# Kernel optimization log

Hardware: AMD Instinct MI355X
Metric: run time of the kernel (lower is better)

Reference implementation:

```python
import jax, jax.numpy as jnp
import numpy as np

B, D, E, H, L = 32768, 512, 10, 128, 2  # batch, input_dim, max_charts, expert hidden, latent_dim
RH1, RH2 = 256, 128                      # router hidden sizes
TAU = 3.0


def setup_inputs() -> dict:
    key = jax.random.key(0)
    ks = jax.random.split(key, 16)
    rnd = lambda k, *s: (jax.random.normal(k, s, jnp.float32) * 0.05)
    return {
        "x": jax.random.normal(ks[0], (B, D), jnp.float32),
        "u": jax.random.uniform(ks[1], (B, E), jnp.float32),
        # router params (last layer init ~ N(0, 0.01), bias 0, as in _init_router)
        "rw1": rnd(ks[2], D, RH1), "rb1": jnp.zeros((RH1,), jnp.float32),
        "rw2": rnd(ks[3], RH1, RH2), "rb2": jnp.zeros((RH2,), jnp.float32),
        "rw3": jax.random.normal(ks[4], (RH2, E), jnp.float32) * 0.01,
        "rb3": jnp.zeros((E,), jnp.float32),
        # stacked expert params: all 10 experts batched along leading dim
        "ew1": rnd(ks[5], E, D, H), "eb1": rnd(ks[6], E, H),
        "ew2": rnd(ks[7], E, H, H), "eb2": rnd(ks[8], E, H),
        "ew3": rnd(ks[9], E, H, L), "eb3": rnd(ks[10], E, L),
    }


def reference(x, u, rw1, rb1, rw2, rb2, rw3, rb3, ew1, eb1, ew2, eb2, ew3, eb3):
    # router MLP: D -> 256 -> 128 -> E
    h = jax.nn.relu(x @ rw1 + rb1)
    h = jax.nn.relu(h @ rw2 + rb2)
    logits = h @ rw3 + rb3                                  # [B, E]
    # gumbel_softmax(tau=3.0, hard=False): softmax((logits + gumbel)/tau)
    g = -jnp.log(-jnp.log(jnp.clip(u, 1e-10, 1.0)) + 1e-10)
    weights = jax.nn.softmax((logits + g) / TAU, axis=1)    # [B, E]
    # all 10 experts as batched GEMMs (fuses the python loop over charts)
    h1 = jax.nn.relu(jnp.einsum('bi,eio->beo', x, ew1) + eb1[None])   # [B, E, H]
    h2 = jax.nn.relu(jnp.einsum('beh,eho->beo', h1, ew2) + eb2[None]) # [B, E, H]
    zc = jnp.einsum('beh,ehl->bel', h2, ew3) + eb3[None]              # [B, E, L]
    z = jnp.einsum('be,bel->bl', weights, zc)                         # [B, L]
    chart_outputs = jnp.transpose(zc, (1, 0, 2))                      # [E, B, L]
    return z, weights, chart_outputs
```

## Files before the change

kernel.cpp:

```cpp
#include <hip/hip_runtime.h>
#include <stdint.h>

typedef __bf16 bf16x8 __attribute__((ext_vector_type(8)));
typedef float floatx4 __attribute__((ext_vector_type(4)));
typedef unsigned short ushort_t;

__device__ __forceinline__ ushort_t bf16rne(float f) {
    union { float f; unsigned u; } v; v.f = f;
    return (ushort_t)((v.u + 0x7fffu + ((v.u >> 16) & 1u)) >> 16);
}

__device__ __forceinline__ void gl_lds16(const ushort_t* g, ushort_t* l) {
    __builtin_amdgcn_global_load_lds(
        (const __attribute__((address_space(1))) unsigned int*)g,
        (__attribute__((address_space(3))) unsigned int*)l, 16, 0, 0);
}


#define WAIT_VM_BAR(n)    do { asm volatile("s_waitcnt vmcnt(" #n ")" ::: "memory"); __builtin_amdgcn_s_barrier(); } while (0)
#define WAIT_VM_LG_BAR(n) do { asm volatile("s_waitcnt vmcnt(" #n ") lgkmcnt(0)" ::: "memory"); __builtin_amdgcn_s_barrier(); } while (0)
#define WAIT_LG_BAR()     do { asm volatile("s_waitcnt lgkmcnt(0)" ::: "memory"); __builtin_amdgcn_s_barrier(); } while (0)

__global__ void prep(const float* __restrict__ x, ushort_t* __restrict__ x16,
                     const float* __restrict__ ew1, ushort_t* __restrict__ ew1t,
                     const float* __restrict__ ew2, ushort_t* __restrict__ ew2t,
                     const float* __restrict__ rw1, ushort_t* __restrict__ rw1t,
                     const float* __restrict__ rw2, ushort_t* __restrict__ rw2t) {
    __shared__ ushort_t sT[64 * 65];
    int b = blockIdx.x, tid = threadIdx.x;
    if (b < 16384) {
        int i = b * 256 + tid;
        float4 f = ((const float4*)x)[i];
        union { ushort_t s[4]; uint2 v; } pk;
        pk.s[0] = bf16rne(f.x); pk.s[1] = bf16rne(f.y);
        pk.s[2] = bf16rne(f.z); pk.s[3] = bf16rne(f.w);
        ((uint2*)x16)[i] = pk.v;
        return;
    }
    const float* in; ushort_t* outp; int K, N, k0, n0;
    int i = b - 16384;
    if (i < 160) {
        int e = i >> 4, t = i & 15;
        in = ew1 + e * 65536; outp = ew1t + e * 65536;
        K = 512; N = 128; k0 = (t >> 1) * 64; n0 = (t & 1) * 64;
    } else if (i < 200) {
        i -= 160; int e = i >> 2, t = i & 3;
        in = ew2 + e * 16384; outp = ew2t + e * 16384;
        K = 128; N = 128; k0 = (t >> 1) * 64; n0 = (t & 1) * 64;
    } else if (i < 232) {
        i -= 200; in = rw1; outp = rw1t;
        K = 512; N = 256; k0 = (i >> 2) * 64; n0 = (i & 3) * 64;
    } else {
        i -= 232; in = rw2; outp = rw2t;
        K = 256; N = 128; k0 = (i >> 1) * 64; n0 = (i & 1) * 64;
    }
    {
        int c = tid & 63, r0 = tid >> 6;
#pragma unroll
        for (int p = 0; p < 16; ++p) {
            int r = r0 * 16 + p;
            sT[c * 65 + r] = bf16rne(in[(size_t)(k0 + r) * N + n0 + c]);
        }
        __syncthreads();
        int rr = tid & 63, c0 = tid >> 6;
#pragma unroll
        for (int p = 0; p < 16; ++p) {
            int cc = c0 * 16 + p;
            outp[(size_t)(n0 + cc) * K + k0 + rr] = sT[cc * 65 + rr];
        }
    }
}

__global__ __launch_bounds__(256, 2)
void fused_main(const ushort_t* __restrict__ x16,
                const ushort_t* __restrict__ rw1t, const float* __restrict__ rb1,
                const ushort_t* __restrict__ rw2t, const float* __restrict__ rb2,
                const float* __restrict__ rw3, const float* __restrict__ rb3,
                const float* __restrict__ u,
                const ushort_t* __restrict__ ew1t, const ushort_t* __restrict__ ew2t,
                const float* __restrict__ eb1, const float* __restrict__ eb2,
                const float* __restrict__ ew3, const float* __restrict__ eb3,
                float* __restrict__ wts, float* __restrict__ chart) {
    __shared__ alignas(16) ushort_t sU[24576];
    __shared__ float sB1[2][128];
    __shared__ float sB2[2][128];
    __shared__ float sW3e[2][256];
    __shared__ float zbuf[128][2];

    const int tid = threadIdx.x;
    const int id = blockIdx.x;
    const int wave = tid >> 6, lane = tid & 63;
    const int ln15 = lane & 15, q = lane >> 4;
    const int wm = (wave & 1) * 64, wn = (wave >> 1) * 64;
    const int mhalf = wm >> 6, nhalf = wn >> 6;
    const int rl = lane >> 2, cl = lane & 3;
    const int sw = (cl ^ ((rl >> 1) & 3)) * 8;
    const int rg0 = wave * 2, rg1 = rg0 + 1;
    const int fslot = (4 * ln15 + (q ^ ((ln15 >> 1) & 3))) * 8;

    if (id < 256) {
        const int rb = (id & 7) * 32 + (id >> 3);
        if (tid < 128) sB2[0][tid] = rb2[tid];
        else sB2[1][tid - 128] = rb2[tid];
        const ushort_t* xblk = x16 + (size_t)rb * 128 * 512;

        const ushort_t* w1base = rw1t;
        auto stage_rt = [&](int dst, int k0) {
            gl_lds16(xblk + (size_t)(rg0 * 16 + rl) * 512 + k0 + sw, &sU[dst + rg0 * 512]);
            gl_lds16(xblk + (size_t)(rg1 * 16 + rl) * 512 + k0 + sw, &sU[dst + rg1 * 512]);
            gl_lds16(w1base + (size_t)(rg0 * 16 + rl) * 512 + k0 + sw, &sU[dst + 4096 + rg0 * 512]);
            gl_lds16(w1base + (size_t)(rg1 * 16 + rl) * 512 + k0 + sw, &sU[dst + 4096 + rg1 * 512]);
        };
        auto stage_rw2 = [&](int dst, int kh, int ph) {
#pragma unroll
            for (int r = 0; r < 2; ++r) {
                int s = wave * 2 + r;
                gl_lds16(rw2t + (size_t)(s * 16 + rl) * 256 + ph * 128 + kh * 32 + sw,
                         &sU[dst + s * 512]);
            }
        };

        floatx4 acc2[4][4];
#pragma unroll
        for (int i = 0; i < 4; ++i)
#pragma unroll
            for (int j = 0; j < 4; ++j) acc2[i][j] = (floatx4){0.f, 0.f, 0.f, 0.f};

        auto comp_rg2 = [&](int rbase, int kh) {
            bf16x8 a[4], b[4];
#pragma unroll
            for (int t = 0; t < 4; ++t) a[t] = *(const bf16x8*)(&sU[rbase + (mhalf * 4 + t) * 512 + fslot]);
#pragma unroll
            for (int t = 0; t < 4; ++t) b[t] = *(const bf16x8*)(&sU[8192 + kh * 4096 + (nhalf * 4 + t) * 512 + lane * 8]);
            __builtin_amdgcn_s_setprio(1);
#pragma unroll
            for (int i = 0; i < 4; ++i)
#pragma unroll
                for (int j = 0; j < 4; ++j)
                    acc2[i][j] = __builtin_amdgcn_mfma_f32_16x16x32_bf16(a[i], b[j], acc2[i][j], 0, 0, 0);
            __builtin_amdgcn_s_setprio(0);
        };

        for (int ph = 0; ph < 2; ++ph) {
            w1base = rw1t + (size_t)ph * 65536;
            if (tid < 128) sB1[0][tid] = rb1[ph * 128 + tid];

            floatx4 acc[4][4];
#pragma unroll
            for (int i = 0; i < 4; ++i)
#pragma unroll
                for (int j = 0; j < 4; ++j) acc[i][j] = (floatx4){0.f, 0.f, 0.f, 0.f};

            auto comp_rt = [&](int base) {
                bf16x8 a[4], b[4];
#pragma unroll
                for (int t = 0; t < 4; ++t) a[t] = *(const bf16x8*)(&sU[base + 4096 + (mhalf * 4 + t) * 512 + fslot]);
#pragma unroll
                for (int t = 0; t < 4; ++t) b[t] = *(const bf16x8*)(&sU[base + (nhalf * 4 + t) * 512 + fslot]);
                __builtin_amdgcn_s_setprio(1);
#pragma unroll
                for (int i = 0; i < 4; ++i)
#pragma unroll
                    for (int j = 0; j < 4; ++j)
                        acc[i][j] = __builtin_amdgcn_mfma_f32_16x16x32_bf16(a[i], b[j], acc[i][j], 0, 0, 0);
                __builtin_amdgcn_s_setprio(0);
            };

            stage_rt(0, 0);
#pragma unroll 1
            for (int p = 0; p < 8; ++p) {
                int k0 = p * 64;
                stage_rt(8192, k0 + 32);
                WAIT_VM_BAR(4);
                comp_rt(0);
                WAIT_LG_BAR();
                if (p < 7) {
                    stage_rt(0, k0 + 64);
                    WAIT_VM_BAR(4);
                } else {
                    WAIT_VM_BAR(0);
                }
                comp_rt(8192);
                WAIT_LG_BAR();
            }

            stage_rw2(0, 0, ph);

#pragma unroll
            for (int i = 0; i < 4; ++i) {
                int hbase = wm + 16 * i;
                int kh = hbase >> 5;
                int qhi = (hbase >> 4) & 1;
                int slotq = 2 * qhi + (q >> 1);
                int h0 = hbase + q * 4;
#pragma unroll
                for (int j = 0; j < 4; ++j) {
                    union { ushort_t s[4]; uint2 v; } pk;
#pragma unroll
                    for (int r = 0; r < 4; ++r)
                        pk.s[r] = bf16rne(fmaxf(acc[i][j][r] + sB1[0][h0 + r], 0.f));
                    *(uint2*)(&sU[8192 + kh * 4096 + (nhalf * 4 + j) * 512 + slotq * 128 + ln15 * 8 + (q & 1) * 4]) = pk.v;
                }
            }

            stage_rw2(4096, 1, ph); WAIT_VM_LG_BAR(8); comp_rg2(0, 0);    WAIT_LG_BAR();
            stage_rw2(0, 2, ph);    WAIT_VM_LG_BAR(8); comp_rg2(4096, 1); WAIT_LG_BAR();
            stage_rw2(4096, 3, ph); WAIT_VM_LG_BAR(8); comp_rg2(0, 2);    WAIT_LG_BAR();
            WAIT_VM_LG_BAR(0);                         comp_rg2(4096, 3); WAIT_LG_BAR();
        }

        __syncthreads();
        float* sw3r = (float*)sU;
        float* lgbuf = (float*)(&sU[2560]);
        for (int i = tid; i < 1280; i += 256) sw3r[i] = rw3[i];
        __syncthreads();

        float lg[4][10];
#pragma unroll
        for (int j = 0; j < 4; ++j)
#pragma unroll
            for (int ee = 0; ee < 10; ++ee) lg[j][ee] = 0.f;
#pragma unroll
        for (int i = 0; i < 4; ++i) {
#pragma unroll
            for (int r = 0; r < 4; ++r) {
                int n = wm + i * 16 + q * 4 + r;
                float bias = n < 128 ? sB2[0][n] : sB2[1][n - 128];
                const float* w3r = &sw3r[n * 10];
#pragma unroll
                for (int j = 0; j < 4; ++j) {
                    float val = fmaxf(acc2[i][j][r] + bias, 0.f);
#pragma unroll
                    for (int ee = 0; ee < 10; ++ee) lg[j][ee] += val * w3r[ee];
                }
            }
        }
#pragma unroll
        for (int j = 0; j < 4; ++j)
#pragma unroll
            for (int ee = 0; ee < 10; ++ee) {
                lg[j][ee] += __shfl_xor(lg[j][ee], 16, 64);
                lg[j][ee] += __shfl_xor(lg[j][ee], 32, 64);
            }
        if (wm == 0 && q == 0) {
#pragma unroll
            for (int j = 0; j < 4; ++j) {
                int row = wn + 16 * j + ln15;
#pragma unroll
                for (int ee = 0; ee < 10; ++ee) lgbuf[row * 10 + ee] = lg[j][ee];
            }
        }
        __syncthreads();
        if (wm == 64 && q == 0) {
#pragma unroll
            for (int j = 0; j < 4; ++j) {
                int row = wn + 16 * j + ln15;
#pragma unroll
                for (int ee = 0; ee < 10; ++ee) lgbuf[row * 10 + ee] += lg[j][ee];
            }
        }
        __syncthreads();
        if (tid < 128) {
            int grow = rb * 128 + tid;
            float v[10], mx = -1e30f;
#pragma unroll
            for (int ee = 0; ee < 10; ++ee) {
                float uu = u[(size_t)grow * 10 + ee];
                uu = fminf(fmaxf(uu, 1e-10f), 1.0f);
                float g = -logf(-logf(uu) + 1e-10f);
                v[ee] = (lgbuf[tid * 10 + ee] + rb3[ee] + g) * (1.0f / 3.0f);
                mx = fmaxf(mx, v[ee]);
            }
            float s = 0.f;
#pragma unroll
            for (int ee = 0; ee < 10; ++ee) { v[ee] = expf(v[ee] - mx); s += v[ee]; }
            float inv = 1.0f / s;
#pragma unroll
            for (int ee = 0; ee < 10; ++ee) wts[(size_t)grow * 10 + ee] = v[ee] * inv;
        }
    } else {
        const int eid = id - 256;
        const int xcd = eid & 7, local = eid >> 3;
        const int pr = local % 5;
        const int rb = xcd * 32 + local / 5;
        const int e0 = pr * 2;

        if (tid < 128) {
            sB1[0][tid] = eb1[e0 * 128 + tid];
            sB2[0][tid] = eb2[e0 * 128 + tid];
        } else {
            sB1[1][tid - 128] = eb1[(e0 + 1) * 128 + (tid - 128)];
            sB2[1][tid - 128] = eb2[(e0 + 1) * 128 + (tid - 128)];
        }
        sW3e[0][tid] = ew3[e0 * 256 + tid];
        sW3e[1][tid] = ew3[(e0 + 1) * 256 + tid];

        const ushort_t* xblk = x16 + (size_t)rb * 128 * 512;
        const ushort_t* w1a = ew1t + (size_t)e0 * 65536;
        const ushort_t* w1b = w1a + 65536;

        floatx4 accA[4][4], accB[4][4];
#pragma unroll
        for (int i = 0; i < 4; ++i)
#pragma unroll
            for (int j = 0; j < 4; ++j) {
                accA[i][j] = (floatx4){0.f, 0.f, 0.f, 0.f};
                accB[i][j] = (floatx4){0.f, 0.f, 0.f, 0.f};
            }

        auto stage_g1 = [&](int dst, int k0) {
            gl_lds16(xblk + (size_t)(rg0 * 16 + rl) * 512 + k0 + sw, &sU[dst + rg0 * 512]);
            gl_lds16(xblk + (size_t)(rg1 * 16 + rl) * 512 + k0 + sw, &sU[dst + rg1 * 512]);
            gl_lds16(w1a + (size_t)(rg0 * 16 + rl) * 512 + k0 + sw, &sU[dst + 4096 + rg0 * 512]);
            gl_lds16(w1a + (size_t)(rg1 * 16 + rl) * 512 + k0 + sw, &sU[dst + 4096 + rg1 * 512]);
            gl_lds16(w1b + (size_t)(rg0 * 16 + rl) * 512 + k0 + sw, &sU[dst + 8192 + rg0 * 512]);
            gl_lds16(w1b + (size_t)(rg1 * 16 + rl) * 512 + k0 + sw, &sU[dst + 8192 + rg1 * 512]);
        };
        auto comp_g1 = [&](int base) {
            bf16x8 a0[4], a1[4], b[4];
#pragma unroll
            for (int t = 0; t < 4; ++t) b[t] = *(const bf16x8*)(&sU[base + (nhalf * 4 + t) * 512 + fslot]);
#pragma unroll
            for (int t = 0; t < 4; ++t) a0[t] = *(const bf16x8*)(&sU[base + 4096 + (mhalf * 4 + t) * 512 + fslot]);
#pragma unroll
            for (int t = 0; t < 4; ++t) a1[t] = *(const bf16x8*)(&sU[base + 8192 + (mhalf * 4 + t) * 512 + fslot]);
            __builtin_amdgcn_s_setprio(1);
#pragma unroll
            for (int i = 0; i < 4; ++i)
#pragma unroll
                for (int j = 0; j < 4; ++j) {
                    accA[i][j] = __builtin_amdgcn_mfma_f32_16x16x32_bf16(a0[i], b[j], accA[i][j], 0, 0, 0);
                    accB[i][j] = __builtin_amdgcn_mfma_f32_16x16x32_bf16(a1[i], b[j], accB[i][j], 0, 0, 0);
                }
            __builtin_amdgcn_s_setprio(0);
        };

        stage_g1(0, 0);
#pragma unroll 1
        for (int p = 0; p < 8; ++p) {
            int k0 = p * 64;
            stage_g1(12288, k0 + 32);
            WAIT_VM_BAR(6);
            comp_g1(0);
            WAIT_LG_BAR();
            if (p < 7) {
                stage_g1(0, k0 + 64);
                WAIT_VM_BAR(6);
            } else {
                WAIT_VM_BAR(0);
            }
            comp_g1(12288);
            WAIT_LG_BAR();
        }

        auto stage_w2 = [&](const ushort_t* w2, int dst, int kh) {
#pragma unroll
            for (int r = 0; r < 2; ++r) {
                int s = wave * 2 + r;
                gl_lds16(w2 + (size_t)(s * 16 + rl) * 128 + kh * 32 + sw, &sU[dst + s * 512]);
            }
        };
        auto comp_g2 = [&](int rbase, int kh, floatx4 (&acc2)[4][4]) {
            bf16x8 a[4], b[4];
#pragma unroll
            for (int t = 0; t < 4; ++t) a[t] = *(const bf16x8*)(&sU[rbase + (mhalf * 4 + t) * 512 + fslot]);
#pragma unroll
            for (int t = 0; t < 4; ++t) b[t] = *(const bf16x8*)(&sU[8192 + kh * 4096 + (nhalf * 4 + t) * 512 + lane * 8]);
            __builtin_amdgcn_s_setprio(1);
#pragma unroll
            for (int i = 0; i < 4; ++i)
#pragma unroll
                for (int j = 0; j < 4; ++j)
                    acc2[i][j] = __builtin_amdgcn_mfma_f32_16x16x32_bf16(a[i], b[j], acc2[i][j], 0, 0, 0);
            __builtin_amdgcn_s_setprio(0);
        };

#pragma unroll
        for (int ex = 0; ex < 2; ++ex) {
            const int e = e0 + ex;
            const ushort_t* w2 = ew2t + (size_t)e * 16384;

            stage_w2(w2, 0, 0);

#pragma unroll
            for (int i = 0; i < 4; ++i) {
                int hbase = wm + 16 * i;
                int kh = hbase >> 5;
                int qhi = (hbase >> 4) & 1;
                int slotq = 2 * qhi + (q >> 1);
                int h0 = hbase + q * 4;
#pragma unroll
                for (int j = 0; j < 4; ++j) {
                    union { ushort_t s[4]; uint2 v; } pk;
#pragma unroll
                    for (int r = 0; r < 4; ++r) {
                        float av = ex == 0 ? accA[i][j][r] : accB[i][j][r];
                        pk.s[r] = bf16rne(fmaxf(av + sB1[ex][h0 + r], 0.f));
                    }
                    *(uint2*)(&sU[8192 + kh * 4096 + (nhalf * 4 + j) * 512 + slotq * 128 + ln15 * 8 + (q & 1) * 4]) = pk.v;
                }
            }

            floatx4 acc2[4][4];
#pragma unroll
            for (int i = 0; i < 4; ++i)
#pragma unroll
                for (int j = 0; j < 4; ++j) acc2[i][j] = (floatx4){0.f, 0.f, 0.f, 0.f};

            stage_w2(w2, 4096, 1); WAIT_VM_LG_BAR(8); comp_g2(0, 0, acc2);    WAIT_LG_BAR();
            stage_w2(w2, 0, 2);    WAIT_VM_LG_BAR(8); comp_g2(4096, 1, acc2); WAIT_LG_BAR();
            stage_w2(w2, 4096, 3); WAIT_VM_LG_BAR(8); comp_g2(0, 2, acc2);    WAIT_LG_BAR();
            WAIT_VM_LG_BAR(0);                        comp_g2(4096, 3, acc2); WAIT_LG_BAR();

            float zc0[4] = {0.f, 0.f, 0.f, 0.f}, zc1[4] = {0.f, 0.f, 0.f, 0.f};
#pragma unroll
            for (int i = 0; i < 4; ++i) {
                int o0 = wm + i * 16 + q * 4;
#pragma unroll
                for (int r = 0; r < 4; ++r) {
                    int o = o0 + r;
                    float w3a = sW3e[ex][2 * o], w3b = sW3e[ex][2 * o + 1];
                    float bias = sB2[ex][o];
#pragma unroll
                    for (int j = 0; j < 4; ++j) {
                        float val = fmaxf(acc2[i][j][r] + bias, 0.f);
                        zc0[j] += val * w3a;
                        zc1[j] += val * w3b;
                    }
                }
            }
#pragma unroll
            for (int j = 0; j < 4; ++j) {
                zc0[j] += __shfl_xor(zc0[j], 16, 64);
                zc0[j] += __shfl_xor(zc0[j], 32, 64);
                zc1[j] += __shfl_xor(zc1[j], 16, 64);
                zc1[j] += __shfl_xor(zc1[j], 32, 64);
            }
            if (wm == 0 && q == 0) {
#pragma unroll
                for (int j = 0; j < 4; ++j) {
                    int row = wn + j * 16 + ln15;
                    zbuf[row][0] = zc0[j];
                    zbuf[row][1] = zc1[j];
                }
            }
            __syncthreads();
            if (wm == 64 && q == 0) {
#pragma unroll
                for (int j = 0; j < 4; ++j) {
                    int row = wn + j * 16 + ln15;
                    zbuf[row][0] += zc0[j];
                    zbuf[row][1] += zc1[j];
                }
            }
            __syncthreads();
            {
                int row = tid >> 1, l = tid & 1;
                int grow = rb * 128 + row;
                chart[(size_t)e * 65536 + (size_t)grow * 2 + l] = zbuf[row][l] + eb3[e * 2 + l];
            }
        }
    }
}

__global__ void z_final(const float* __restrict__ w, const float* __restrict__ chart,
                        float* __restrict__ z) {
    int row = blockIdx.x * 256 + threadIdx.x;
    float z0 = 0.f, z1 = 0.f;
#pragma unroll
    for (int e = 0; e < 10; ++e) {
        float we = w[(size_t)row * 10 + e];
        float2 c = *(const float2*)(&chart[(size_t)e * 65536 + (size_t)row * 2]);
        z0 += we * c.x;
        z1 += we * c.y;
    }
    float2 o; o.x = z0; o.y = z1;
    *(float2*)(&z[(size_t)row * 2]) = o;
}

extern "C" void kernel_launch(void* const* d_in, const int* in_sizes, int n_in,
                              void* d_out, int out_size, void* d_ws, size_t ws_size,
                              hipStream_t stream) {
    const float* x = (const float*)d_in[0];
    const float* u = (const float*)d_in[1];
    const float* rw1 = (const float*)d_in[2];
    const float* rb1 = (const float*)d_in[3];
    const float* rw2 = (const float*)d_in[4];
    const float* rb2 = (const float*)d_in[5];
    const float* rw3 = (const float*)d_in[6];
    const float* rb3 = (const float*)d_in[7];
    const float* ew1 = (const float*)d_in[8];
    const float* eb1 = (const float*)d_in[9];
    const float* ew2 = (const float*)d_in[10];
    const float* eb2 = (const float*)d_in[11];
    const float* ew3 = (const float*)d_in[12];
    const float* eb3 = (const float*)d_in[13];
    float* out = (float*)d_out;
    float* z = out;
    float* wts = out + 65536;
    float* chart = out + 393216;

    ushort_t* x16  = (ushort_t*)d_ws;
    ushort_t* ew1t = x16 + 16777216;
    ushort_t* ew2t = ew1t + 655360;
    ushort_t* rw1t = ew2t + 163840;
    ushort_t* rw2t = rw1t + 131072;

    prep<<<16624, 256, 0, stream>>>(x, x16, ew1, ew1t, ew2, ew2t, rw1, rw1t, rw2, rw2t);

    fused_main<<<1536, 256, 0, stream>>>(x16, rw1t, rb1, rw2t, rb2, rw3, rb3, u,
                                         ew1t, ew2t, eb1, eb2, ew3, eb3,
                                         wts, chart);

    z_final<<<128, 256, 0, stream>>>(wts, chart, z);
}
```

Before: 204.4 us.

## Fuse fp32-to-bf16 conversion of x into the main kernel's staging pipeline

Drops the prep pass that converted x to a bf16 workspace copy. The main kernel now loads fp32 x into registers, converts it, and writes bf16 into LDS inside the software pipeline, while the weights still go through direct global-to-LDS loads. This removes a full write and read of a 32 MB bf16 copy of x. In exchange, each expert-pair block reads fp32 x, twice the bytes, and holds more registers, which may lower occupancy. Wait counts are retuned, one barrier is removed, and z_final now stages the weights through shared memory.

```diff
diff --git a/kernel.cpp b/kernel.cpp
--- a/kernel.cpp
+++ b/kernel.cpp
@@ -17,28 +17,18 @@
 }
 
 
-#define WAIT_VM_BAR(n)    do { asm volatile("s_waitcnt vmcnt(" #n ")" ::: "memory"); __builtin_amdgcn_s_barrier(); } while (0)
+#define WAIT_VM(n)        asm volatile("s_waitcnt vmcnt(" #n ")" ::: "memory")
 #define WAIT_VM_LG_BAR(n) do { asm volatile("s_waitcnt vmcnt(" #n ") lgkmcnt(0)" ::: "memory"); __builtin_amdgcn_s_barrier(); } while (0)
 #define WAIT_LG_BAR()     do { asm volatile("s_waitcnt lgkmcnt(0)" ::: "memory"); __builtin_amdgcn_s_barrier(); } while (0)
 
-__global__ void prep(const float* __restrict__ x, ushort_t* __restrict__ x16,
-                     const float* __restrict__ ew1, ushort_t* __restrict__ ew1t,
+__global__ void prep(const float* __restrict__ ew1, ushort_t* __restrict__ ew1t,
                      const float* __restrict__ ew2, ushort_t* __restrict__ ew2t,
                      const float* __restrict__ rw1, ushort_t* __restrict__ rw1t,
                      const float* __restrict__ rw2, ushort_t* __restrict__ rw2t) {
     __shared__ ushort_t sT[64 * 65];
-    int b = blockIdx.x, tid = threadIdx.x;
-    if (b < 16384) {
-        int i = b * 256 + tid;
-        float4 f = ((const float4*)x)[i];
-        union { ushort_t s[4]; uint2 v; } pk;
-        pk.s[0] = bf16rne(f.x); pk.s[1] = bf16rne(f.y);
-        pk.s[2] = bf16rne(f.z); pk.s[3] = bf16rne(f.w);
-        ((uint2*)x16)[i] = pk.v;
-        return;
-    }
+    int tid = threadIdx.x;
     const float* in; ushort_t* outp; int K, N, k0, n0;
-    int i = b - 16384;
+    int i = blockIdx.x;
     if (i < 160) {
         int e = i >> 4, t = i & 15;
         in = ew1 + e * 65536; outp = ew1t + e * 65536;
@@ -72,7 +62,7 @@
 }
 
 __global__ __launch_bounds__(256, 2)
-void fused_main(const ushort_t* __restrict__ x16,
+void fused_main(const float* __restrict__ xf,
                 const ushort_t* __restrict__ rw1t, const float* __restrict__ rb1,
                 const ushort_t* __restrict__ rw2t, const float* __restrict__ rb2,
                 const float* __restrict__ rw3, const float* __restrict__ rb3,
@@ -98,16 +88,34 @@
     const int rg0 = wave * 2, rg1 = rg0 + 1;
     const int fslot = (4 * ln15 + (q ^ ((ln15 >> 1) & 3))) * 8;
 
+    float4 xv0, xv1, xv2, xv3;
+    const int xw0 = rg0 * 512 + rl * 32 + sw;
+    const int xw1 = rg1 * 512 + rl * 32 + sw;
+
     if (id < 256) {
         const int rb = (id & 7) * 32 + (id >> 3);
         if (tid < 128) sB2[0][tid] = rb2[tid];
         else sB2[1][tid - 128] = rb2[tid];
-        const ushort_t* xblk = x16 + (size_t)rb * 128 * 512;
+        const float* xblk = xf + (size_t)rb * 128 * 512;
+        const float* xg0 = xblk + (size_t)(rg0 * 16 + rl) * 512 + cl * 8;
+        const float* xg1 = xblk + (size_t)(rg1 * 16 + rl) * 512 + cl * 8;
+
+        auto xload = [&](int k0) {
+            xv0 = *(const float4*)(xg0 + k0); xv1 = *(const float4*)(xg0 + k0 + 4);
+            xv2 = *(const float4*)(xg1 + k0); xv3 = *(const float4*)(xg1 + k0 + 4);
+        };
+        auto cvt_write = [&](int dst) {
+            bf16x8 o0, o1;
+            o0[0] = (__bf16)xv0.x; o0[1] = (__bf16)xv0.y; o0[2] = (__bf16)xv0.z; o0[3] = (__bf16)xv0.w;
+            o0[4] = (__bf16)xv1.x; o0[5] = (__bf16)xv1.y; o0[6] = (__bf16)xv1.z; o0[7] = (__bf16)xv1.w;
+            o1[0] = (__bf16)xv2.x; o1[1] = (__bf16)xv2.y; o1[2] = (__bf16)xv2.z; o1[3] = (__bf16)xv2.w;
+            o1[4] = (__bf16)xv3.x; o1[5] = (__bf16)xv3.y; o1[6] = (__bf16)xv3.z; o1[7] = (__bf16)xv3.w;
+            *(bf16x8*)(&sU[dst + xw0]) = o0;
+            *(bf16x8*)(&sU[dst + xw1]) = o1;
+        };
 
         const ushort_t* w1base = rw1t;
-        auto stage_rt = [&](int dst, int k0) {
-            gl_lds16(xblk + (size_t)(rg0 * 16 + rl) * 512 + k0 + sw, &sU[dst + rg0 * 512]);
-            gl_lds16(xblk + (size_t)(rg1 * 16 + rl) * 512 + k0 + sw, &sU[dst + rg1 * 512]);
+        auto stage_rw1 = [&](int dst, int k0) {
             gl_lds16(w1base + (size_t)(rg0 * 16 + rl) * 512 + k0 + sw, &sU[dst + 4096 + rg0 * 512]);
             gl_lds16(w1base + (size_t)(rg1 * 16 + rl) * 512 + k0 + sw, &sU[dst + 4096 + rg1 * 512]);
         };
@@ -166,23 +174,30 @@
                 __builtin_amdgcn_s_setprio(0);
             };
 
-            stage_rt(0, 0);
+            xload(0);
+            stage_rw1(0, 0);
+            WAIT_VM(2);
+            cvt_write(0);
+            xload(32);
+            WAIT_VM_LG_BAR(4);
 #pragma unroll 1
-            for (int p = 0; p < 8; ++p) {
+            for (int p = 0; p < 7; ++p) {
                 int k0 = p * 64;
-                stage_rt(8192, k0 + 32);
-                WAIT_VM_BAR(4);
+                stage_rw1(8192, k0 + 32);
+                WAIT_VM(2); cvt_write(8192); xload(k0 + 64);
                 comp_rt(0);
-                WAIT_LG_BAR();
-                if (p < 7) {
-                    stage_rt(0, k0 + 64);
-                    WAIT_VM_BAR(4);
-                } else {
-                    WAIT_VM_BAR(0);
-                }
+                WAIT_VM_LG_BAR(4);
+                stage_rw1(0, k0 + 64);
+                WAIT_VM(2); cvt_write(0); xload(k0 + 96);
                 comp_rt(8192);
-                WAIT_LG_BAR();
-            }
+                WAIT_VM_LG_BAR(4);
+            }
+            stage_rw1(8192, 480);
+            WAIT_VM(2); cvt_write(8192);
+            comp_rt(0);
+            WAIT_VM_LG_BAR(0);
+            comp_rt(8192);
+            WAIT_LG_BAR();
 
             stage_rw2(0, 0, ph);
 
@@ -203,13 +218,12 @@
                 }
             }
 
-            stage_rw2(4096, 1, ph); WAIT_VM_LG_BAR(8); comp_rg2(0, 0);    WAIT_LG_BAR();
-            stage_rw2(0, 2, ph);    WAIT_VM_LG_BAR(8); comp_rg2(4096, 1); WAIT_LG_BAR();
-            stage_rw2(4096, 3, ph); WAIT_VM_LG_BAR(8); comp_rg2(0, 2);    WAIT_LG_BAR();
+            stage_rw2(4096, 1, ph); WAIT_VM_LG_BAR(2); comp_rg2(0, 0);    WAIT_LG_BAR();
+            stage_rw2(0, 2, ph);    WAIT_VM_LG_BAR(2); comp_rg2(4096, 1); WAIT_LG_BAR();
+            stage_rw2(4096, 3, ph); WAIT_VM_LG_BAR(2); comp_rg2(0, 2);
             WAIT_VM_LG_BAR(0);                         comp_rg2(4096, 3); WAIT_LG_BAR();
         }
 
-        __syncthreads();
         float* sw3r = (float*)sU;
         float* lgbuf = (float*)(&sU[2560]);
         for (int i = tid; i < 1280; i += 256) sw3r[i] = rw3[i];
@@ -295,27 +309,41 @@
         sW3e[0][tid] = ew3[e0 * 256 + tid];
         sW3e[1][tid] = ew3[(e0 + 1) * 256 + tid];
 
-        const ushort_t* xblk = x16 + (size_t)rb * 128 * 512;
+        const float* xblk = xf + (size_t)rb * 128 * 512;
+        const float* xg0 = xblk + (size_t)(rg0 * 16 + rl) * 512 + cl * 8;
+        const float* xg1 = xblk + (size_t)(rg1 * 16 + rl) * 512 + cl * 8;
         const ushort_t* w1a = ew1t + (size_t)e0 * 65536;
         const ushort_t* w1b = w1a + 65536;
 
-        floatx4 accA[4][4], accB[4][4];
-#pragma unroll
-        for (int i = 0; i < 4; ++i)
-#pragma unroll
-            for (int j = 0; j < 4; ++j) {
-                accA[i][j] = (floatx4){0.f, 0.f, 0.f, 0.f};
-                accB[i][j] = (floatx4){0.f, 0.f, 0.f, 0.f};
-            }
-
-        auto stage_g1 = [&](int dst, int k0) {
-            gl_lds16(xblk + (size_t)(rg0 * 16 + rl) * 512 + k0 + sw, &sU[dst + rg0 * 512]);
-            gl_lds16(xblk + (size_t)(rg1 * 16 + rl) * 512 + k0 + sw, &sU[dst + rg1 * 512]);
+        auto xload = [&](int k0) {
+            xv0 = *(const float4*)(xg0 + k0); xv1 = *(const float4*)(xg0 + k0 + 4);
+            xv2 = *(const float4*)(xg1 + k0); xv3 = *(const float4*)(xg1 + k0 + 4);
+        };
+        auto cvt_write = [&](int dst) {
+            bf16x8 o0, o1;
+            o0[0] = (__bf16)xv0.x; o0[1] = (__bf16)xv0.y; o0[2] = (__bf16)xv0.z; o0[3] = (__bf16)xv0.w;
+            o0[4] = (__bf16)xv1.x; o0[5] = (__bf16)xv1.y; o0[6] = (__bf16)xv1.z; o0[7] = (__bf16)xv1.w;
+            o1[0] = (__bf16)xv2.x; o1[1] = (__bf16)xv2.y; o1[2] = (__bf16)xv2.z; o1[3] = (__bf16)xv2.w;
+            o1[4] = (__bf16)xv3.x; o1[5] = (__bf16)xv3.y; o1[6] = (__bf16)xv3.z; o1[7] = (__bf16)xv3.w;
+            *(bf16x8*)(&sU[dst + xw0]) = o0;
+            *(bf16x8*)(&sU[dst + xw1]) = o1;
+        };
+        auto stage_w1 = [&](int dst, int k0) {
             gl_lds16(w1a + (size_t)(rg0 * 16 + rl) * 512 + k0 + sw, &sU[dst + 4096 + rg0 * 512]);
             gl_lds16(w1a + (size_t)(rg1 * 16 + rl) * 512 + k0 + sw, &sU[dst + 4096 + rg1 * 512]);
             gl_lds16(w1b + (size_t)(rg0 * 16 + rl) * 512 + k0 + sw, &sU[dst + 8192 + rg0 * 512]);
             gl_lds16(w1b + (size_t)(rg1 * 16 + rl) * 512 + k0 + sw, &sU[dst + 8192 + rg1 * 512]);
         };
+
+        floatx4 accA[4][4], accB[4][4];
+#pragma unroll
+        for (int i = 0; i < 4; ++i)
+#pragma unroll
+            for (int j = 0; j < 4; ++j) {
+                accA[i][j] = (floatx4){0.f, 0.f, 0.f, 0.f};
+                accB[i][j] = (floatx4){0.f, 0.f, 0.f, 0.f};
+            }
+
         auto comp_g1 = [&](int base) {
             bf16x8 a0[4], a1[4], b[4];
 #pragma unroll
@@ -335,23 +363,30 @@
             __builtin_amdgcn_s_setprio(0);
         };
 
-        stage_g1(0, 0);
+        xload(0);
+        stage_w1(0, 0);
+        WAIT_VM(4);
+        cvt_write(0);
+        xload(32);
+        WAIT_VM_LG_BAR(4);
 #pragma unroll 1
-        for (int p = 0; p < 8; ++p) {
+        for (int p = 0; p < 7; ++p) {
             int k0 = p * 64;
-            stage_g1(12288, k0 + 32);
-            WAIT_VM_BAR(6);
+            stage_w1(12288, k0 + 32);
+            WAIT_VM(4); cvt_write(12288); xload(k0 + 64);
             comp_g1(0);
-            WAIT_LG_BAR();
-            if (p < 7) {
-                stage_g1(0, k0 + 64);
-                WAIT_VM_BAR(6);
-            } else {
-                WAIT_VM_BAR(0);
-            }
+            WAIT_VM_LG_BAR(4);
+            stage_w1(0, k0 + 64);
+            WAIT_VM(4); cvt_write(0); xload(k0 + 96);
             comp_g1(12288);
-            WAIT_LG_BAR();
-        }
+            WAIT_VM_LG_BAR(4);
+        }
+        stage_w1(12288, 480);
+        WAIT_VM(4); cvt_write(12288);
+        comp_g1(0);
+        WAIT_VM_LG_BAR(0);
+        comp_g1(12288);
+        WAIT_LG_BAR();
 
         auto stage_w2 = [&](const ushort_t* w2, int dst, int kh) {
 #pragma unroll
@@ -407,9 +442,9 @@
 #pragma unroll
                 for (int j = 0; j < 4; ++j) acc2[i][j] = (floatx4){0.f, 0.f, 0.f, 0.f};
 
-            stage_w2(w2, 4096, 1); WAIT_VM_LG_BAR(8); comp_g2(0, 0, acc2);    WAIT_LG_BAR();
-            stage_w2(w2, 0, 2);    WAIT_VM_LG_BAR(8); comp_g2(4096, 1, acc2); WAIT_LG_BAR();
-            stage_w2(w2, 4096, 3); WAIT_VM_LG_BAR(8); comp_g2(0, 2, acc2);    WAIT_LG_BAR();
+            stage_w2(w2, 4096, 1); WAIT_VM_LG_BAR(2); comp_g2(0, 0, acc2);    WAIT_LG_BAR();
+            stage_w2(w2, 0, 2);    WAIT_VM_LG_BAR(2); comp_g2(4096, 1, acc2); WAIT_LG_BAR();
+            stage_w2(w2, 4096, 3); WAIT_VM_LG_BAR(2); comp_g2(0, 2, acc2);
             WAIT_VM_LG_BAR(0);                        comp_g2(4096, 3, acc2); WAIT_LG_BAR();
 
             float zc0[4] = {0.f, 0.f, 0.f, 0.f}, zc1[4] = {0.f, 0.f, 0.f, 0.f};
@@ -465,11 +500,15 @@
 
 __global__ void z_final(const float* __restrict__ w, const float* __restrict__ chart,
                         float* __restrict__ z) {
-    int row = blockIdx.x * 256 + threadIdx.x;
+    __shared__ float swt[2560];
+    int b0 = blockIdx.x * 256;
+    for (int i = threadIdx.x; i < 2560; i += 256) swt[i] = w[(size_t)b0 * 10 + i];
+    __syncthreads();
+    int row = b0 + threadIdx.x;
     float z0 = 0.f, z1 = 0.f;
 #pragma unroll
     for (int e = 0; e < 10; ++e) {
-        float we = w[(size_t)row * 10 + e];
+        float we = swt[threadIdx.x * 10 + e];
         float2 c = *(const float2*)(&chart[(size_t)e * 65536 + (size_t)row * 2]);
         z0 += we * c.x;
         z1 += we * c.y;
@@ -500,15 +539,14 @@
     float* wts = out + 65536;
     float* chart = out + 393216;
 
-    ushort_t* x16  = (ushort_t*)d_ws;
-    ushort_t* ew1t = x16 + 16777216;
+    ushort_t* ew1t = (ushort_t*)d_ws;
     ushort_t* ew2t = ew1t + 655360;
     ushort_t* rw1t = ew2t + 163840;
     ushort_t* rw2t = rw1t + 131072;
 
-    prep<<<16624, 256, 0, stream>>>(x, x16, ew1, ew1t, ew2, ew2t, rw1, rw1t, rw2, rw2t);
-
-    fused_main<<<1536, 256, 0, stream>>>(x16, rw1t, rb1, rw2t, rb2, rw3, rb3, u,
+    prep<<<240, 256, 0, stream>>>(ew1, ew1t, ew2, ew2t, rw1, rw1t, rw2, rw2t);
+
+    fused_main<<<1536, 256, 0, stream>>>(x, rw1t, rb1, rw2t, rb2, rw3, rb3, u,
                                          ew1t, ew2t, eb1, eb2, ew3, eb3,
                                          wts, chart);
 
```

Result: slower. 216.0 us (+5.7%).

## Restructure double-buffered GEMM pipelines to one barrier per stage and prefetch next expert

Applied to the files above, without the earlier changes.

The router and expert GEMM loops now issue the next LDS stage, compute the current buffer, and then do a single full vmcnt/lgkmcnt wait plus barrier. This replaces the earlier pattern of partial-count waits with two barriers per step. The first W2 tile for each expert is prefetched during the tail of the previous computation, and one __syncthreads after the router phase is removed. z_final now stages the gumbel weights through shared memory so the global reads are coalesced. Waiting for all loads to finish (vmcnt 0) removes some of the load/compute overlap that partial counts allowed, and dropping the syncthreads could introduce a race.

```diff
diff --git a/kernel.cpp b/kernel.cpp
--- a/kernel.cpp
+++ b/kernel.cpp
@@ -17,7 +17,6 @@
 }
 
 
-#define WAIT_VM_BAR(n)    do { asm volatile("s_waitcnt vmcnt(" #n ")" ::: "memory"); __builtin_amdgcn_s_barrier(); } while (0)
 #define WAIT_VM_LG_BAR(n) do { asm volatile("s_waitcnt vmcnt(" #n ") lgkmcnt(0)" ::: "memory"); __builtin_amdgcn_s_barrier(); } while (0)
 #define WAIT_LG_BAR()     do { asm volatile("s_waitcnt lgkmcnt(0)" ::: "memory"); __builtin_amdgcn_s_barrier(); } while (0)
 
@@ -104,8 +103,7 @@
         else sB2[1][tid - 128] = rb2[tid];
         const ushort_t* xblk = x16 + (size_t)rb * 128 * 512;
 
-        const ushort_t* w1base = rw1t;
-        auto stage_rt = [&](int dst, int k0) {
+        auto stage_rt = [&](int dst, int k0, const ushort_t* w1base) {
             gl_lds16(xblk + (size_t)(rg0 * 16 + rl) * 512 + k0 + sw, &sU[dst + rg0 * 512]);
             gl_lds16(xblk + (size_t)(rg1 * 16 + rl) * 512 + k0 + sw, &sU[dst + rg1 * 512]);
             gl_lds16(w1base + (size_t)(rg0 * 16 + rl) * 512 + k0 + sw, &sU[dst + 4096 + rg0 * 512]);
@@ -142,7 +140,7 @@
         };
 
         for (int ph = 0; ph < 2; ++ph) {
-            w1base = rw1t + (size_t)ph * 65536;
+            const ushort_t* w1base = rw1t + (size_t)ph * 65536;
             if (tid < 128) sB1[0][tid] = rb1[ph * 128 + tid];
 
             floatx4 acc[4][4];
@@ -166,25 +164,23 @@
                 __builtin_amdgcn_s_setprio(0);
             };
 
-            stage_rt(0, 0);
+            stage_rt(0, 0, w1base);
+            WAIT_VM_LG_BAR(0);
 #pragma unroll 1
             for (int p = 0; p < 8; ++p) {
                 int k0 = p * 64;
-                stage_rt(8192, k0 + 32);
-                WAIT_VM_BAR(4);
+                stage_rt(8192, k0 + 32, w1base);
                 comp_rt(0);
-                WAIT_LG_BAR();
+                WAIT_VM_LG_BAR(0);
                 if (p < 7) {
-                    stage_rt(0, k0 + 64);
-                    WAIT_VM_BAR(4);
-                } else {
-                    WAIT_VM_BAR(0);
-                }
-                comp_rt(8192);
-                WAIT_LG_BAR();
-            }
-
+                    stage_rt(0, k0 + 64, w1base);
+                    comp_rt(8192);
+                    WAIT_VM_LG_BAR(0);
+                }
+            }
             stage_rw2(0, 0, ph);
+            comp_rt(8192);
+            WAIT_LG_BAR();
 
 #pragma unroll
             for (int i = 0; i < 4; ++i) {
@@ -203,13 +199,14 @@
                 }
             }
 
-            stage_rw2(4096, 1, ph); WAIT_VM_LG_BAR(8); comp_rg2(0, 0);    WAIT_LG_BAR();
-            stage_rw2(0, 2, ph);    WAIT_VM_LG_BAR(8); comp_rg2(4096, 1); WAIT_LG_BAR();
-            stage_rw2(4096, 3, ph); WAIT_VM_LG_BAR(8); comp_rg2(0, 2);    WAIT_LG_BAR();
-            WAIT_VM_LG_BAR(0);                         comp_rg2(4096, 3); WAIT_LG_BAR();
-        }
-
-        __syncthreads();
+            WAIT_VM_LG_BAR(0);
+            stage_rw2(4096, 1, ph); comp_rg2(0, 0);    WAIT_VM_LG_BAR(0);
+            stage_rw2(0, 2, ph);    comp_rg2(4096, 1); WAIT_VM_LG_BAR(0);
+            stage_rw2(4096, 3, ph); comp_rg2(0, 2);    WAIT_VM_LG_BAR(0);
+            comp_rg2(4096, 3);
+            WAIT_LG_BAR();
+        }
+
         float* sw3r = (float*)sU;
         float* lgbuf = (float*)(&sU[2560]);
         for (int i = tid; i < 1280; i += 256) sw3r[i] = rw3[i];
@@ -334,53 +331,50 @@
                 }
             __builtin_amdgcn_s_setprio(0);
         };
+        auto stage_w2 = [&](const ushort_t* w2, int dst, int kh) {
+#pragma unroll
+            for (int r = 0; r < 2; ++r) {
+                int s = wave * 2 + r;
+                gl_lds16(w2 + (size_t)(s * 16 + rl) * 128 + kh * 32 + sw, &sU[dst + s * 512]);
+            }
+        };
+        auto comp_g2 = [&](int rbase, int kh, floatx4 (&acc2)[4][4]) {
+            bf16x8 a[4], b[4];
+#pragma unroll
+            for (int t = 0; t < 4; ++t) a[t] = *(const bf16x8*)(&sU[rbase + (mhalf * 4 + t) * 512 + fslot]);
+#pragma unroll
+            for (int t = 0; t < 4; ++t) b[t] = *(const bf16x8*)(&sU[8192 + kh * 4096 + (nhalf * 4 + t) * 512 + lane * 8]);
+            __builtin_amdgcn_s_setprio(1);
+#pragma unroll
+            for (int i = 0; i < 4; ++i)
+#pragma unroll
+                for (int j = 0; j < 4; ++j)
+                    acc2[i][j] = __builtin_amdgcn_mfma_f32_16x16x32_bf16(a[i], b[j], acc2[i][j], 0, 0, 0);
+            __builtin_amdgcn_s_setprio(0);
+        };
 
         stage_g1(0, 0);
+        WAIT_VM_LG_BAR(0);
 #pragma unroll 1
         for (int p = 0; p < 8; ++p) {
             int k0 = p * 64;
             stage_g1(12288, k0 + 32);
-            WAIT_VM_BAR(6);
             comp_g1(0);
-            WAIT_LG_BAR();
+            WAIT_VM_LG_BAR(0);
             if (p < 7) {
                 stage_g1(0, k0 + 64);
-                WAIT_VM_BAR(6);
-            } else {
-                WAIT_VM_BAR(0);
-            }
-            comp_g1(12288);
-            WAIT_LG_BAR();
-        }
-
-        auto stage_w2 = [&](const ushort_t* w2, int dst, int kh) {
-#pragma unroll
-            for (int r = 0; r < 2; ++r) {
-                int s = wave * 2 + r;
-                gl_lds16(w2 + (size_t)(s * 16 + rl) * 128 + kh * 32 + sw, &sU[dst + s * 512]);
-            }
-        };
-        auto comp_g2 = [&](int rbase, int kh, floatx4 (&acc2)[4][4]) {
-            bf16x8 a[4], b[4];
-#pragma unroll
-            for (int t = 0; t < 4; ++t) a[t] = *(const bf16x8*)(&sU[rbase + (mhalf * 4 + t) * 512 + fslot]);
-#pragma unroll
-            for (int t = 0; t < 4; ++t) b[t] = *(const bf16x8*)(&sU[8192 + kh * 4096 + (nhalf * 4 + t) * 512 + lane * 8]);
-            __builtin_amdgcn_s_setprio(1);
-#pragma unroll
-            for (int i = 0; i < 4; ++i)
-#pragma unroll
-                for (int j = 0; j < 4; ++j)
-                    acc2[i][j] = __builtin_amdgcn_mfma_f32_16x16x32_bf16(a[i], b[j], acc2[i][j], 0, 0, 0);
-            __builtin_amdgcn_s_setprio(0);
-        };
+                comp_g1(12288);
+                WAIT_VM_LG_BAR(0);
+            }
+        }
+        stage_w2(ew2t + (size_t)e0 * 16384, 0, 0);
+        comp_g1(12288);
+        WAIT_LG_BAR();
 
 #pragma unroll
         for (int ex = 0; ex < 2; ++ex) {
             const int e = e0 + ex;
             const ushort_t* w2 = ew2t + (size_t)e * 16384;
-
-            stage_w2(w2, 0, 0);
 
 #pragma unroll
             for (int i = 0; i < 4; ++i) {
@@ -407,10 +401,12 @@
 #pragma unroll
                 for (int j = 0; j < 4; ++j) acc2[i][j] = (floatx4){0.f, 0.f, 0.f, 0.f};
 
-            stage_w2(w2, 4096, 1); WAIT_VM_LG_BAR(8); comp_g2(0, 0, acc2);    WAIT_LG_BAR();
-            stage_w2(w2, 0, 2);    WAIT_VM_LG_BAR(8); comp_g2(4096, 1, acc2); WAIT_LG_BAR();
-            stage_w2(w2, 4096, 3); WAIT_VM_LG_BAR(8); comp_g2(0, 2, acc2);    WAIT_LG_BAR();
-            WAIT_VM_LG_BAR(0);                        comp_g2(4096, 3, acc2); WAIT_LG_BAR();
+            WAIT_VM_LG_BAR(0);
+            stage_w2(w2, 4096, 1); comp_g2(0, 0, acc2);    WAIT_VM_LG_BAR(0);
+            stage_w2(w2, 0, 2);    comp_g2(4096, 1, acc2); WAIT_VM_LG_BAR(0);
+            stage_w2(w2, 4096, 3); comp_g2(0, 2, acc2);    WAIT_VM_LG_BAR(0);
+            if (ex == 0) stage_w2(ew2t + (size_t)(e0 + 1) * 16384, 0, 0);
+            comp_g2(4096, 3, acc2);
 
             float zc0[4] = {0.f, 0.f, 0.f, 0.f}, zc1[4] = {0.f, 0.f, 0.f, 0.f};
 #pragma unroll
@@ -465,11 +461,15 @@
 
 __global__ void z_final(const float* __restrict__ w, const float* __restrict__ chart,
                         float* __restrict__ z) {
-    int row = blockIdx.x * 256 + threadIdx.x;
+    __shared__ float swt[2560];
+    int b0 = blockIdx.x * 256;
+    for (int i = threadIdx.x; i < 2560; i += 256) swt[i] = w[(size_t)b0 * 10 + i];
+    __syncthreads();
+    int row = b0 + threadIdx.x;
     float z0 = 0.f, z1 = 0.f;
 #pragma unroll
     for (int e = 0; e < 10; ++e) {
-        float we = w[(size_t)row * 10 + e];
+        float we = swt[threadIdx.x * 10 + e];
         float2 c = *(const float2*)(&chart[(size_t)e * 65536 + (size_t)row * 2]);
         z0 += we * c.x;
         z1 += we * c.y;
```

Result: no change. 205.8 us (+0.7%).
